# Kernel tuning notes

Measured on AMD Instinct MI355X. Metric: run time of the kernel, lower is better.

## Reference

```python
import jax, jax.numpy as jnp
import numpy as np

N = 16384   # total nodes per drug-batch
E = 65536   # directed edges (avg degree 4)
B = 512     # graphs per batch
BN_EPS = 1e-5
SLOPE = 0.01  # LeakyReLU default


def _rn(k, shape, s=0.02):
    return jax.random.normal(k, shape, dtype=jnp.float32) * s


def setup_inputs():
    key = jax.random.key(0)
    ks = jax.random.split(key, 32)
    d = {}
    d['x1'] = jax.random.normal(ks[0], (N, 78), dtype=jnp.float32)
    d['edge_index1'] = jax.random.randint(ks[1], (2, E), 0, N)
    d['batch1'] = jnp.sort(jax.random.randint(ks[2], (N,), 0, B))
    d['x2'] = jax.random.normal(ks[3], (N, 78), dtype=jnp.float32)
    d['edge_index2'] = jax.random.randint(ks[4], (2, E), 0, N)
    d['batch2'] = jnp.sort(jax.random.randint(ks[5], (N,), 0, B))
    d['cell'] = jax.random.normal(ks[6], (B, 954), dtype=jnp.float32)
    # TransformerConv1: 78 -> 2 heads x 128 (concat 256)
    d['wq1'] = _rn(ks[7], (78, 256));  d['bq1'] = jnp.zeros((256,), jnp.float32)
    d['wk1'] = _rn(ks[8], (78, 256));  d['bk1'] = jnp.zeros((256,), jnp.float32)
    d['wv1'] = _rn(ks[9], (78, 256));  d['bv1'] = jnp.zeros((256,), jnp.float32)
    d['ws1'] = _rn(ks[10], (78, 256)); d['bs1'] = jnp.zeros((256,), jnp.float32)
    # TransformerConv2: 256 -> 2 heads x 512 (concat 1024)
    d['wq2'] = _rn(ks[11], (256, 1024)); d['bq2'] = jnp.zeros((1024,), jnp.float32)
    d['wk2'] = _rn(ks[12], (256, 1024)); d['bk2'] = jnp.zeros((1024,), jnp.float32)
    d['wv2'] = _rn(ks[13], (256, 1024)); d['bv2'] = jnp.zeros((1024,), jnp.float32)
    d['ws2'] = _rn(ks[14], (256, 1024)); d['bs2'] = jnp.zeros((1024,), jnp.float32)
    d['wg1'] = _rn(ks[15], (1024, 512)); d['bg1'] = jnp.zeros((512,), jnp.float32)
    d['wg2'] = _rn(ks[16], (512, 128));  d['bg2'] = jnp.zeros((128,), jnp.float32)
    d['wr1'] = _rn(ks[17], (954, 512));  d['br1'] = jnp.zeros((512,), jnp.float32)
    d['wr2'] = _rn(ks[18], (512, 256));  d['br2'] = jnp.zeros((256,), jnp.float32)
    d['wr3'] = _rn(ks[19], (256, 128));  d['br3'] = jnp.zeros((128,), jnp.float32)
    d['wf1'] = _rn(ks[20], (384, 512));  d['bf1'] = jnp.zeros((512,), jnp.float32)
    d['gbn1'] = jnp.ones((512,), jnp.float32); d['bbn1'] = jnp.zeros((512,), jnp.float32)
    d['wf2'] = _rn(ks[21], (512, 256));  d['bf2'] = jnp.zeros((256,), jnp.float32)
    d['gbn2'] = jnp.ones((256,), jnp.float32); d['bbn2'] = jnp.zeros((256,), jnp.float32)
    d['wf3'] = _rn(ks[22], (256, 1));    d['bf3'] = jnp.zeros((1,), jnp.float32)
    return d


def _lrelu(x):
    return jnp.where(x >= 0, x, SLOPE * x)


def _l2n(x):
    return x / jnp.maximum(jnp.linalg.norm(x, axis=1, keepdims=True), 1e-12)


def _tconv(x, ei, wq, bq, wk, bk, wv, bv, ws, bs, H, D):
    # PyG TransformerConv (concat=True, beta=False, root_weight=True)
    src, dst = ei[0], ei[1]
    n = x.shape[0]
    q = (x @ wq + bq).reshape(n, H, D)
    k = (x @ wk + bk).reshape(n, H, D)
    v = (x @ wv + bv).reshape(n, H, D)
    logits = jnp.einsum('ehd,ehd->eh', q[dst], k[src]) / jnp.sqrt(jnp.float32(D))  # [E,H]
    m = jax.ops.segment_max(logits, dst, num_segments=n)
    m = jnp.where(jnp.isfinite(m), m, 0.0)
    e = jnp.exp(logits - m[dst])
    z = jax.ops.segment_sum(e, dst, num_segments=n)
    alpha = e / (z[dst] + 1e-16)
    agg = jax.ops.segment_sum(alpha[:, :, None] * v[src], dst, num_segments=n)  # [N,H,D]
    return agg.reshape(n, H * D) + x @ ws + bs


def reference(x1, edge_index1, batch1, x2, edge_index2, batch2, cell,
              wq1, bq1, wk1, bk1, wv1, bv1, ws1, bs1,
              wq2, bq2, wk2, bk2, wv2, bv2, ws2, bs2,
              wg1, bg1, wg2, bg2, wr1, br1, wr2, br2, wr3, br3,
              wf1, bf1, gbn1, bbn1, wf2, bf2, gbn2, bbn2, wf3, bf3):
    def branch(x, ei, bt):
        h = _lrelu(_tconv(x, ei, wq1, bq1, wk1, bk1, wv1, bv1, ws1, bs1, 2, 128))
        h = _lrelu(_tconv(h, ei, wq2, bq2, wk2, bk2, wv2, bv2, ws2, bs2, 2, 512))
        g = jax.ops.segment_max(h, bt, num_segments=B)  # global max pool per graph
        g = jnp.where(jnp.isfinite(g), g, 0.0)
        g = _lrelu(g @ wg1 + bg1)
        g = g @ wg2 + bg2  # dropout = identity in eval
        return _l2n(g)

    x1g = branch(x1, edge_index1, batch1)
    x2g = branch(x2, edge_index2, batch2)

    c = _l2n(cell)
    c = _lrelu(c @ wr1 + br1)
    c = _lrelu(c @ wr2 + br2)
    c = c @ wr3 + br3

    xc = _l2n(jnp.concatenate([x1g, x2g, c], axis=1))  # [B, 384]
    bn = 1.0 / jnp.sqrt(1.0 + BN_EPS)  # eval BN with running mean 0, var 1
    h = _lrelu((xc @ wf1 + bf1) * bn * gbn1 + bbn1)
    h = _lrelu((h @ wf2 + bf2) * bn * gbn2 + bbn2)
    return jax.nn.sigmoid((h @ wf3 + bf3)[:, 0])
```

## Files before the change

kernel.cpp:

```cpp
#include <hip/hip_runtime.h>
#include <hip/hip_bf16.h>
#include <hip/hip_fp8.h>
#include <math.h>
#include <stdint.h>

typedef __hip_bfloat16 bf16;

#define NN 16384
#define EE 65536
#define BB 512

typedef __attribute__((ext_vector_type(8))) short short8;
typedef __attribute__((ext_vector_type(2))) short short2v;
typedef __attribute__((ext_vector_type(4))) float floatx4;
typedef __attribute__((ext_vector_type(2))) float floatx2;
typedef __attribute__((ext_vector_type(2))) unsigned int uint2v;

#define GKEY_NEGINF 0x007FFFFFu

__device__ __forceinline__ float lrelu_f(float x){ return x >= 0.f ? x : 0.01f*x; }

__device__ __forceinline__ float b2f(short s){
    unsigned int u = ((unsigned int)(unsigned short)s) << 16;
    float f; __builtin_memcpy(&f, &u, 4); return f;
}
__device__ __forceinline__ short f2b(float f){
    bf16 b = (bf16)f;
    short s; __builtin_memcpy(&s, &b, 2); return s;
}
__device__ __forceinline__ unsigned int fkey(float f){
    unsigned int u; __builtin_memcpy(&u, &f, 4);
    return (u & 0x80000000u) ? ~u : (u | 0x80000000u);
}
__device__ __forceinline__ float fdec(unsigned int k){
    if (k == GKEY_NEGINF) return 0.f;
    unsigned int u = (k & 0x80000000u) ? (k ^ 0x80000000u) : ~k;
    float f; __builtin_memcpy(&f, &u, 4); return f;
}

__device__ __forceinline__ void gl2lds16(const void* g, void* l){
    __builtin_amdgcn_global_load_lds(
        (__attribute__((address_space(1))) unsigned int*)(uintptr_t)g,
        (__attribute__((address_space(3))) unsigned int*)(uintptr_t)l, 16, 0, 0);
}

__global__ __launch_bounds__(256)
void mfma_gemm(const bf16* __restrict__ A, int lda,
               const bf16* __restrict__ Bt, int ldb,
               const float* __restrict__ bias,
               bf16* __restrict__ C, int ldc,
               unsigned char* __restrict__ C2, int ldc2, int nsplit, int K)
{
    __shared__ __align__(16) char smem[20480];
    bf16* As  = (bf16*)smem;
    bf16* Bs  = (bf16*)(smem + 8192);
    bf16* epi = (bf16*)smem;
    const int tid  = threadIdx.x;
    const int wave = tid >> 6;
    const int lane = tid & 63;
    const int wm = (wave & 1) * 64;
    const int wn = (wave >> 1) * 64;
    const int m0 = blockIdx.x * 128;
    const int n0 = blockIdx.y * 128;
    const bool isf8 = (n0 >= nsplit);

    const int srow = lane >> 2;
    const int scol = (((lane & 3) ^ ((srow >> 1) & 3))) * 8;
    const int arow = lane & 15;
    const int aq   = (((lane >> 4) ^ ((arow >> 1) & 3))) * 8;

    floatx4 acc[4][4];
    #pragma unroll
    for (int i=0;i<4;i++)
        #pragma unroll
        for (int j=0;j<4;j++) acc[i][j] = (floatx4){0.f,0.f,0.f,0.f};

    for (int k0 = 0; k0 < K; k0 += 32) {
        #pragma unroll
        for (int i = 0; i < 2; i++) {
            const int chunk = wave*2 + i;
            const int r = chunk*16 + srow;
            gl2lds16(A  + (size_t)(m0 + r)*lda + k0 + scol, As + chunk*512);
            gl2lds16(Bt + (size_t)(n0 + r)*ldb + k0 + scol, Bs + chunk*512);
        }
        __syncthreads();
        short8 af[4], bf_[4];
        #pragma unroll
        for (int i=0;i<4;i++) af[i]  = *(const short8*)(As + (wm + i*16 + arow)*32 + aq);
        #pragma unroll
        for (int j=0;j<4;j++) bf_[j] = *(const short8*)(Bs + (wn + j*16 + arow)*32 + aq);
        #pragma unroll
        for (int i=0;i<4;i++)
            #pragma unroll
            for (int j=0;j<4;j++)
                acc[i][j] = __builtin_amdgcn_mfma_f32_16x16x32_bf16(af[i], bf_[j], acc[i][j], 0,0,0);
        __syncthreads();
    }
    const int crow = (lane >> 4) * 4;
    const int ccol = lane & 15;
    const int erow = lane >> 2;
    const int ecol = (lane & 3) * 8;
    bf16* ep = epi + wave * (64*40);
    #pragma unroll
    for (int j2 = 0; j2 < 2; j2++){
        if (j2) __syncthreads();
        #pragma unroll
        for (int jj = 0; jj < 2; jj++){
            const int j = j2*2 + jj;
            const float bsv = bias[n0 + wn + j*16 + ccol];
            #pragma unroll
            for (int i = 0; i < 4; i++)
                #pragma unroll
                for (int r = 0; r < 4; r++)
                    ep[(i*16 + crow + r)*40 + jj*16 + ccol] = (bf16)(acc[i][j][r] + bsv);
        }
        __syncthreads();
        #pragma unroll
        for (int q = 0; q < 4; q++){
            const int rr = q*16 + erow;
            short8 vv = *(const short8*)(ep + rr*40 + ecol);
            if (!isf8){
                *(short8*)(C + (size_t)(m0 + wm + rr)*ldc + n0 + wn + j2*32 + ecol) = vv;
            } else {
                int d0 = 0, d1 = 0;
                d0 = __builtin_amdgcn_cvt_pk_fp8_f32(b2f(vv[0]), b2f(vv[1]), d0, false);
                d0 = __builtin_amdgcn_cvt_pk_fp8_f32(b2f(vv[2]), b2f(vv[3]), d0, true);
                d1 = __builtin_amdgcn_cvt_pk_fp8_f32(b2f(vv[4]), b2f(vv[5]), d1, false);
                d1 = __builtin_amdgcn_cvt_pk_fp8_f32(b2f(vv[6]), b2f(vv[7]), d1, true);
                uint2v ob; ob[0] = (unsigned int)d0; ob[1] = (unsigned int)d1;
                *(uint2v*)(C2 + (size_t)(m0 + wm + rr)*ldc2 + (n0 - nsplit) + wn + j2*32 + ecol) = ob;
            }
        }
    }
}

#define OG1 0
#define OG2 524288
#define OR1 589824
#define OR2 1081344
#define OR3 1212416
#define OF1 1245184
#define OF2 1441792
#define TAILW_TOTAL 1572864

#define P_W1T 98304
#define P_B1C (P_W1T + 1024)
#define P_W2T (P_B1C + 1048576)
#define P_B2C (P_W2T + 4096)
#define P_WTP (P_B2C + TAILW_TOTAL)
#define P_XA  (P_WTP + 2*NN*96)
#define P_GK  (P_XA + 2*BB*1024)
__global__ void prep_mega_kernel(
    const float* __restrict__ wq1, const float* __restrict__ wk1,
    const float* __restrict__ wv1, const float* __restrict__ ws1,
    const float* __restrict__ bq1, const float* __restrict__ bk1,
    const float* __restrict__ bv1, const float* __restrict__ bs1,
    const float* __restrict__ wq2, const float* __restrict__ wk2,
    const float* __restrict__ wv2, const float* __restrict__ ws2,
    const float* __restrict__ bq2, const float* __restrict__ bk2,
    const float* __restrict__ bv2, const float* __restrict__ bs2v,
    const float* __restrict__ wg1, const float* __restrict__ wg2,
    const float* __restrict__ wr1, const float* __restrict__ wr2,
    const float* __restrict__ wr3, const float* __restrict__ wf1,
    const float* __restrict__ wf2,
    const float* __restrict__ x1,  const float* __restrict__ x2,
    bf16* __restrict__ W1t, float* __restrict__ b1c,
    bf16* __restrict__ W2t, float* __restrict__ b2c,
    bf16* __restrict__ Wtp, bf16* __restrict__ xa,
    unsigned int* __restrict__ gkey)
{
    int i = blockIdx.x*256 + threadIdx.x;
    if (i < P_W1T){
        int n = i / 96, k = i - n*96;
        int seg = n >> 8;
        const float* w = (seg==0)?ws1:(seg==1)?wq1:(seg==2)?wk1:wv1;
        W1t[i] = (k < 78) ? (bf16)w[(size_t)k*256 + (n & 255)] : (bf16)0.f;
        return;
    }
    if (i < P_B1C){
        int n = i - P_W1T;
        int seg = n >> 8;
        const float* b = (seg==0)?bs1:(seg==1)?bq1:(seg==2)?bk1:bv1;
        b1c[n] = b[n & 255];
        return;
    }
    if (i < P_W2T){
        int loc = i - P_B1C;
        int k = loc & 255;
        int j = (loc >> 8) & 2047;
        int h = loc >> 19;
        const float* w = (j<512)?ws2:(j<1024)?wq2:(j<1536)?wk2:wv2;
        W2t[loc] = (bf16)w[(size_t)k*1024 + h*512 + (j & 511)];
        return;
    }
    if (i < P_B2C){
        int loc = i - P_W2T;
        int j = loc & 2047, h = loc >> 11;
        const float* b = (j<512)?bs2v:(j<1024)?bq2:(j<1536)?bk2:bv2;
        b2c[loc] = b[h*512 + (j & 511)];
        return;
    }
    if (i < P_WTP){
        int t = i - P_B2C;
        const float* W; int N, K, KS, base;
        if      (t < OG2){ W = wg1; N = 512; K = 1024; KS = 32; base = OG1; }
        else if (t < OR1){ W = wg2; N = 128; K = 512;  KS = 16; base = OG2; }
        else if (t < OR2){ W = wr1; N = 512; K = 954;  KS = 30; base = OR1; }
        else if (t < OR3){ W = wr2; N = 256; K = 512;  KS = 16; base = OR2; }
        else if (t < OF1){ W = wr3; N = 128; K = 256;  KS = 8;  base = OR3; }
        else if (t < OF2){ W = wf1; N = 512; K = 384;  KS = 12; base = OF1; }
        else             { W = wf2; N = 256; K = 512;  KS = 16; base = OF2; }
        int loc = t - base;
        int j  = loc & 7;
        int ln = (loc >> 3) & 63;
        int rest = loc >> 9;
        int ks = rest % KS;
        int tile = rest / KS;
        int n = tile*16 + (ln & 15);
        int k = ks*32 + (ln >> 4)*8 + j;
        Wtp[t] = (k < K) ? (bf16)W[(size_t)k*N + n] : (bf16)0.f;
        return;
    }
    if (i < P_XA){
        int t = i - P_WTP;
        int r = t / 96, c = t - r*96;
        const float* x = (r >= NN) ? x2 : x1;
        int lr = r & (NN-1);
        xa[t] = (c < 78) ? (bf16)x[(size_t)lr*78 + c] : (bf16)0.f;
        return;
    }
    if (i < P_GK){
        gkey[i - P_XA] = GKEY_NEGINF;
    }
}

__global__ void hist_kernel(const int* __restrict__ ei1, const int* __restrict__ ei2,
                            int* __restrict__ cnt){
    int eg = blockIdx.x*256 + threadIdx.x;
    int br = eg >> 16, e = eg & (EE-1);
    const int* ei = br ? ei2 : ei1;
    atomicAdd(&cnt[br*NN + ei[EE + e]], 1);
}

__global__ __launch_bounds__(1024)
void scan_kernel(const int* __restrict__ hist, int* __restrict__ rowptr,
                 int* __restrict__ rowcur){
    const int br = blockIdx.x;
    hist   += br*NN;
    rowptr += br*(NN+1);
    rowcur += br*(NN+1);
    __shared__ int sums[1024];
    const int t = threadIdx.x;
    const int base = t*16;
    int loc[16]; int s = 0;
    #pragma unroll
    for (int i=0;i<16;i++){ loc[i]=s; s += hist[base+i]; }
    sums[t] = s; __syncthreads();
    for (int o=1;o<1024;o<<=1){
        int v = (t>=o) ? sums[t-o] : 0;
        __syncthreads();
        sums[t] += v;
        __syncthreads();
    }
    int pref = (t>0) ? sums[t-1] : 0;
    #pragma unroll
    for (int i=0;i<16;i++){
        int v = pref + loc[i];
        rowptr[base+i] = v;
        rowcur[base+i] = v;
    }
    if (t==1023) rowptr[NN] = sums[1023];
}

__global__ void scatter_kernel(const int* __restrict__ ei1, const int* __restrict__ ei2,
                               int* __restrict__ rowcur, int* __restrict__ srcs){
    int eg = blockIdx.x*256 + threadIdx.x;
    int br = eg >> 16, e = eg & (EE-1);
    const int* ei = br ? ei2 : ei1;
    int d = ei[EE + e];
    int pos = atomicAdd(&rowcur[br*(NN+1) + d], 1);
    srcs[br*EE + pos] = ei[e];
}

__global__ __launch_bounds__(256)
void attn128_f8(const bf16* __restrict__ s1, const unsigned char* __restrict__ f81,
                bf16* __restrict__ hout,
                const int* __restrict__ rowptr, const int* __restrict__ srcs)
{
    const int lane = threadIdx.x & 63;
    const int gw = blockIdx.x * 4 + (threadIdx.x >> 6);
    const int n = gw >> 1;
    const int h = gw & 1;
    int br = n >> 14;
    int brNN = br*NN, nl = n - brNN;
    rowptr += br*(NN+1); srcs += br*EE;
    const float qscale = rsqrtf(128.f) * 1.44269504f;
    const int hd = h*128 + lane*2;

    unsigned short qw; __builtin_memcpy(&qw, f81 + (size_t)n*768 + hd, 2);
    floatx2 qd = __builtin_amdgcn_cvt_pk_f32_fp8((int)qw, false);
    float qr[2] = { qd[0]*qscale, qd[1]*qscale };

    const int e0 = rowptr[nl], e1 = rowptr[nl+1];
    float m = -INFINITY, z = 0.f;
    float acc[2] = {0.f, 0.f};

    for (int base = e0; base < e1; base += 4){
        const int cnt = min(4, e1 - base);
        int sl = srcs[min(base + (lane & 3), e1 - 1)];
        int src[4];
        #pragma unroll
        for (int j=0;j<4;j++) src[j] = __shfl(sl, j, 64);

        unsigned short kw[4], vw[4];
        #pragma unroll
        for (int j=0;j<4;j++){
            if (j < cnt){
                const unsigned char* rp = f81 + (size_t)(brNN + src[j])*768;
                __builtin_memcpy(&kw[j], rp + 256 + hd, 2);
                __builtin_memcpy(&vw[j], rp + 512 + hd, 2);
            }
        }
        float dt[4];
        #pragma unroll
        for (int j=0;j<4;j++){
            float d = 0.f;
            if (j < cnt){
                floatx2 kd = __builtin_amdgcn_cvt_pk_f32_fp8((int)kw[j], false);
                d = qr[0]*kd[0] + qr[1]*kd[1];
            }
            dt[j] = d;
        }
        #pragma unroll
        for (int o=32;o;o>>=1){
            #pragma unroll
            for (int j=0;j<4;j++) dt[j] += __shfl_xor(dt[j], o, 64);
        }
        float cm = -INFINITY;
        #pragma unroll
        for (int j=0;j<4;j++) if (j < cnt) cm = fmaxf(cm, dt[j]);
        const float mn = fmaxf(m, cm);
        const float cs = exp2f(m - mn);
        z *= cs;
        acc[0] *= cs; acc[1] *= cs;
        #pragma unroll
        for (int j=0;j<4;j++){
            if (j < cnt){
                const float w = exp2f(dt[j] - mn);
                z += w;
                floatx2 vd = __builtin_amdgcn_cvt_pk_f32_fp8((int)vw[j], false);
                acc[0] += w*vd[0];
                acc[1] += w*vd[1];
            }
        }
        m = mn;
    }
    const float invz = 1.0f/(z + 1e-16f);
    const short2v sv = *(const short2v*)(s1 + (size_t)n*256 + hd);
    short2v ov;
    ov[0] = f2b(lrelu_f(b2f(sv[0]) + acc[0]*invz));
    ov[1] = f2b(lrelu_f(b2f(sv[1]) + acc[1]*invz));
    *(short2v*)(hout + (size_t)n*256 + hd) = ov;
}

__global__ __launch_bounds__(256)
void attn512_f8(const bf16* __restrict__ s2, const unsigned char* __restrict__ f82,
                const int* __restrict__ rowptr, const int* __restrict__ srcs,
                const int* __restrict__ bt1, const int* __restrict__ bt2,
                unsigned int* __restrict__ gkey, int gc0)
{
    __shared__ float Sh[4][512];
    __shared__ int Sgid[4];
    const int lane = threadIdx.x & 63;
    const int wave = threadIdx.x >> 6;
    const int n = blockIdx.x * 4 + wave;
    const int br = n >> 14;
    const int brNN = br*NN, nl = n - brNN;
    const int* rp_ = rowptr + br*(NN+1);
    const int* sp_ = srcs + br*EE;
    const float qscale = rsqrtf(512.f) * 1.44269504f;
    const int hd = lane*8;

    float qr[8];
    {
        const uint2v qv = *(const uint2v*)(f82 + (size_t)n*1536 + hd);
        floatx2 a = __builtin_amdgcn_cvt_pk_f32_fp8((int)qv[0], false);
        floatx2 b = __builtin_amdgcn_cvt_pk_f32_fp8((int)qv[0], true);
        floatx2 c = __builtin_amdgcn_cvt_pk_f32_fp8((int)qv[1], false);
        floatx2 d = __builtin_amdgcn_cvt_pk_f32_fp8((int)qv[1], true);
        qr[0]=a[0]*qscale; qr[1]=a[1]*qscale; qr[2]=b[0]*qscale; qr[3]=b[1]*qscale;
        qr[4]=c[0]*qscale; qr[5]=c[1]*qscale; qr[6]=d[0]*qscale; qr[7]=d[1]*qscale;
    }

    const int e0 = rp_[nl], e1 = rp_[nl+1];
    float m = -INFINITY, z = 0.f;
    float acc[8];
    #pragma unroll
    for (int i=0;i<8;i++) acc[i] = 0.f;

    for (int base = e0; base < e1; base += 4){
        const int cnt = min(4, e1 - base);
        int sl = sp_[min(base + (lane & 3), e1 - 1)];
        int src[4];
        #pragma unroll
        for (int j=0;j<4;j++) src[j] = __shfl(sl, j, 64);

        uint2v k2[4], v2[4];
        #pragma unroll
        for (int j=0;j<4;j++){
            if (j < cnt){
                const unsigned char* rp = f82 + (size_t)(brNN + src[j])*1536;
                k2[j] = *(const uint2v*)(rp + 512 + hd);
                v2[j] = *(const uint2v*)(rp + 1024 + hd);
            }
        }
        float dt[4];
        #pragma unroll
        for (int j=0;j<4;j++){
            float d = 0.f;
            if (j < cnt){
                floatx2 p0 = __builtin_amdgcn_cvt_pk_f32_fp8((int)k2[j][0], false);
                floatx2 p1 = __builtin_amdgcn_cvt_pk_f32_fp8((int)k2[j][0], true);
                floatx2 p2 = __builtin_amdgcn_cvt_pk_f32_fp8((int)k2[j][1], false);
                floatx2 p3 = __builtin_amdgcn_cvt_pk_f32_fp8((int)k2[j][1], true);
                d = qr[0]*p0[0] + qr[1]*p0[1] + qr[2]*p1[0] + qr[3]*p1[1]
                  + qr[4]*p2[0] + qr[5]*p2[1] + qr[6]*p3[0] + qr[7]*p3[1];
            }
            dt[j] = d;
        }
        #pragma unroll
        for (int o=32;o;o>>=1){
            #pragma unroll
            for (int j=0;j<4;j++) dt[j] += __shfl_xor(dt[j], o, 64);
        }
        float cm = -INFINITY;
        #pragma unroll
        for (int j=0;j<4;j++) if (j < cnt) cm = fmaxf(cm, dt[j]);
        const float mn = fmaxf(m, cm);
        const float cs = exp2f(m - mn);
        z *= cs;
        #pragma unroll
        for (int i=0;i<8;i++) acc[i] *= cs;
        #pragma unroll
        for (int j=0;j<4;j++){
            if (j < cnt){
                const float w = exp2f(dt[j] - mn);
                z += w;
                floatx2 p0 = __builtin_amdgcn_cvt_pk_f32_fp8((int)v2[j][0], false);
                floatx2 p1 = __builtin_amdgcn_cvt_pk_f32_fp8((int)v2[j][0], true);
                floatx2 p2 = __builtin_amdgcn_cvt_pk_f32_fp8((int)v2[j][1], false);
                floatx2 p3 = __builtin_amdgcn_cvt_pk_f32_fp8((int)v2[j][1], true);
                acc[0] += w*p0[0]; acc[1] += w*p0[1]; acc[2] += w*p1[0]; acc[3] += w*p1[1];
                acc[4] += w*p2[0]; acc[5] += w*p2[1]; acc[6] += w*p3[0]; acc[7] += w*p3[1];
            }
        }
        m = mn;
    }
    const float invz = 1.0f/(z + 1e-16f);
    const short8 sv = *(const short8*)(s2 + (size_t)n*512 + hd);
    #pragma unroll
    for (int i=0;i<8;i++) Sh[wave][hd + i] = lrelu_f(b2f(sv[i]) + acc[i]*invz);
    if (lane == 0) Sgid[wave] = br*BB + (br ? bt2[nl] : bt1[nl]);
    __syncthreads();

    #pragma unroll
    for (int cc=0; cc<2; cc++){
        const int col = threadIdx.x*2 + cc;
        float mx = Sh[0][col];
        int gid = Sgid[0];
        #pragma unroll
        for (int r=1; r<4; r++){
            if (Sgid[r] == gid) mx = fmaxf(mx, Sh[r][col]);
            else {
                atomicMax(&gkey[(size_t)gid*1024 + gc0 + col], fkey(mx));
                gid = Sgid[r]; mx = Sh[r][col];
            }
        }
        atomicMax(&gkey[(size_t)gid*1024 + gc0 + col], fkey(mx));
    }
}

template<int R, int N, int ACT>
__device__ __forceinline__ void dense_mfma(
    const bf16* __restrict__ Wm, const float* __restrict__ bias,
    const float* __restrict__ gam, const float* __restrict__ bet, float bns,
    const float* A, int lda, float* C, int ldc, int K, int tid)
{
    constexpr int T   = N / 16;
    constexpr int TPW = (T + 15) / 16;
    const int wave = tid >> 6;
    const int lane = tid & 63;
    const int am = lane & 15;
    const int ak = (lane >> 4) * 8;
    const int KS = ((K + 31) & ~31) >> 5;

    floatx4 acc[TPW];
    #pragma unroll
    for (int tp=0; tp<TPW; tp++) acc[tp] = (floatx4){0.f,0.f,0.f,0.f};

    for (int ks = 0; ks < KS; ks++){
        short8 af = (short8){0,0,0,0,0,0,0,0};
        if (am < R){
            const float* ap = A + am*lda + ks*32 + ak;
            const floatx4 a0 = *(const floatx4*)ap;
            const floatx4 a1 = *(const floatx4*)(ap + 4);
            af[0]=f2b(a0[0]); af[1]=f2b(a0[1]); af[2]=f2b(a0[2]); af[3]=f2b(a0[3]);
            af[4]=f2b(a1[0]); af[5]=f2b(a1[1]); af[6]=f2b(a1[2]); af[7]=f2b(a1[3]);
        }
        #pragma unroll
        for (int tp=0; tp<TPW; tp++){
            const int tile = wave + tp*16;
            if (tile < T){
                const short8 bfv = *(const short8*)(Wm + ((size_t)(tile*KS + ks))*512 + lane*8);
                acc[tp] = __builtin_amdgcn_mfma_f32_16x16x32_bf16(af, bfv, acc[tp], 0,0,0);
            }
        }
    }
    const int crow = (lane >> 4) * 4;
    const int ccol = lane & 15;
    #pragma unroll
    for (int tp=0; tp<TPW; tp++){
        const int tile = wave + tp*16;
        if (tile < T){
            #pragma unroll
            for (int r=0; r<4; r++){
                const int row = crow + r;
                if (row < R){
                    const int n = tile*16 + ccol;
                    float v = acc[tp][r] + bias[n];
                    if (ACT==1) v = lrelu_f(v);
                    if (ACT==2) v = lrelu_f(v*bns*gam[n] + bet[n]);
                    C[row*ldc + n] = v;
                }
            }
        }
    }
    __syncthreads();
}

__global__ __launch_bounds__(1024)
void tail_kernel(const unsigned int* __restrict__ gkey,
                 const float* __restrict__ cell,
                 const bf16*  __restrict__ Wtp,
                 const float* __restrict__ bg1, const float* __restrict__ bg2,
                 const float* __restrict__ br1, const float* __restrict__ br2,
                 const float* __restrict__ br3,
                 const float* __restrict__ bf1,
                 const float* __restrict__ gbn1, const float* __restrict__ bbn1,
                 const float* __restrict__ bf2,
                 const float* __restrict__ gbn2, const float* __restrict__ bbn2,
                 const float* __restrict__ wf3, const float* __restrict__ bf3,
                 float bns, float* __restrict__ outp)
{
    __shared__ float Sg[4][1024];
    __shared__ float Sgh[4][512];
    __shared__ float Sgout[4][128];
    __shared__ float Scell[2][960];
    __shared__ float Sc1[2][512];
    __shared__ float Sc2[2][256];
    __shared__ float Sc3[2][128];
    __shared__ float Sxc[2][384];
    __shared__ float Sf1[2][512];
    __shared__ float Sf2[2][256];
    __shared__ float inv4[4], invc[2], invx[2];

    const int tid = threadIdx.x;
    const int wv  = tid >> 6;
    const int ln  = tid & 63;
    const int b0  = blockIdx.x * 2;

    {
        int idx = tid*4;
        int r = idx >> 10, c = idx & 1023;
        int lg = r >> 1, br = r & 1;
        const unsigned int* gp = gkey + (size_t)(br*BB + b0 + lg)*1024 + c;
        #pragma unroll
        for (int i=0;i<4;i++) Sg[r][c+i] = fdec(gp[i]);
    }
    for (int idx = tid; idx < 2*954; idx += 1024){
        int r = (idx >= 954) ? 1 : 0;
        int c = idx - r*954;
        Scell[r][c] = cell[(size_t)(b0 + r)*954 + c];
    }
    if (tid < 12){ int r = tid/6; Scell[r][954 + tid%6] = 0.f; }
    __syncthreads();

    if (wv < 2){
        float s = 0.f;
        for (int c = ln; c < 954; c += 64){ float v = Scell[wv][c]; s += v*v; }
        #pragma unroll
        for (int o=32;o;o>>=1) s += __shfl_xor(s, o, 64);
        if (ln == 0) invc[wv] = 1.0f / fmaxf(sqrtf(s), 1e-12f);
    }
    __syncthreads();
    #pragma unroll
    for (int r=0;r<2;r++)
        for (int c = tid; c < 954; c += 1024) Scell[r][c] *= invc[r];
    __syncthreads();

    dense_mfma<4,512,1>(Wtp+OG1, bg1, nullptr, nullptr, 1.f, &Sg[0][0],   1024, &Sgh[0][0],  512, 1024, tid);
    dense_mfma<4,128,0>(Wtp+OG2, bg2, nullptr, nullptr, 1.f, &Sgh[0][0],  512,  &Sgout[0][0],128, 512,  tid);
    dense_mfma<2,512,1>(Wtp+OR1, br1, nullptr, nullptr, 1.f, &Scell[0][0], 960, &Sc1[0][0],  512, 954,  tid);
    dense_mfma<2,256,1>(Wtp+OR2, br2, nullptr, nullptr, 1.f, &Sc1[0][0],   512, &Sc2[0][0],  256, 512,  tid);
    dense_mfma<2,128,0>(Wtp+OR3, br3, nullptr, nullptr, 1.f, &Sc2[0][0],   256, &Sc3[0][0],  128, 256,  tid);

    if (wv < 4){
        float a = Sgout[wv][ln], bq = Sgout[wv][ln+64];
        float s = a*a + bq*bq;
        #pragma unroll
        for (int o=32;o;o>>=1) s += __shfl_xor(s, o, 64);
        if (ln == 0) inv4[wv] = 1.0f / fmaxf(sqrtf(s), 1e-12f);
    }
    __syncthreads();

    if (tid < 768){
        int lg = tid / 384, j = tid - lg*384;
        float v;
        if (j < 128)      v = Sgout[lg*2+0][j]     * inv4[lg*2+0];
        else if (j < 256) v = Sgout[lg*2+1][j-128] * inv4[lg*2+1];
        else              v = Sc3[lg][j-256];
        Sxc[lg][j] = v;
    }
    __syncthreads();
    if (wv < 2){
        float s = 0.f;
        #pragma unroll
        for (int i=0;i<6;i++){ float v = Sxc[wv][ln + i*64]; s += v*v; }
        #pragma unroll
        for (int o=32;o;o>>=1) s += __shfl_xor(s, o, 64);
        if (ln == 0) invx[wv] = 1.0f / fmaxf(sqrtf(s), 1e-12f);
    }
    __syncthreads();
    if (tid < 768){
        int lg = tid / 384, j = tid - lg*384;
        Sxc[lg][j] *= invx[lg];
    }
    __syncthreads();

    dense_mfma<2,512,2>(Wtp+OF1, bf1, gbn1, bbn1, bns, &Sxc[0][0], 384, &Sf1[0][0], 512, 384, tid);
    dense_mfma<2,256,2>(Wtp+OF2, bf2, gbn2, bbn2, bns, &Sf1[0][0], 512, &Sf2[0][0], 256, 512, tid);

    if (wv < 2){
        float s = 0.f;
        #pragma unroll
        for (int i=0;i<4;i++){ int c = ln + i*64; s += Sf2[wv][c]*wf3[c]; }
        #pragma unroll
        for (int o=32;o;o>>=1) s += __shfl_xor(s, o, 64);
        if (ln == 0) outp[b0 + wv] = 1.0f/(1.0f + expf(-(s + bf3[0])));
    }
}

extern "C" void kernel_launch(void* const* d_in, const int* in_sizes, int n_in,
                              void* d_out, int out_size, void* d_ws, size_t ws_size,
                              hipStream_t stream)
{
    const float* x1  = (const float*)d_in[0];
    const int*   ei1 = (const int*)  d_in[1];
    const int*   bt1 = (const int*)  d_in[2];
    const float* x2  = (const float*)d_in[3];
    const int*   ei2 = (const int*)  d_in[4];
    const int*   bt2 = (const int*)  d_in[5];
    const float* cell= (const float*)d_in[6];
    const float* wq1=(const float*)d_in[7];  const float* bq1=(const float*)d_in[8];
    const float* wk1=(const float*)d_in[9];  const float* bk1=(const float*)d_in[10];
    const float* wv1=(const float*)d_in[11]; const float* bv1=(const float*)d_in[12];
    const float* ws1=(const float*)d_in[13]; const float* bs1=(const float*)d_in[14];
    const float* wq2=(const float*)d_in[15]; const float* bq2=(const float*)d_in[16];
    const float* wk2=(const float*)d_in[17]; const float* bk2=(const float*)d_in[18];
    const float* wv2=(const float*)d_in[19]; const float* bv2=(const float*)d_in[20];
    const float* ws2=(const float*)d_in[21]; const float* bs2q=(const float*)d_in[22];
    const float* wg1=(const float*)d_in[23]; const float* bg1=(const float*)d_in[24];
    const float* wg2=(const float*)d_in[25]; const float* bg2=(const float*)d_in[26];
    const float* wr1=(const float*)d_in[27]; const float* br1=(const float*)d_in[28];
    const float* wr2=(const float*)d_in[29]; const float* br2=(const float*)d_in[30];
    const float* wr3=(const float*)d_in[31]; const float* br3=(const float*)d_in[32];
    const float* wf1=(const float*)d_in[33]; const float* bf1=(const float*)d_in[34];
    const float* gbn1=(const float*)d_in[35];const float* bbn1=(const float*)d_in[36];
    const float* wf2=(const float*)d_in[37]; const float* bf2=(const float*)d_in[38];
    const float* gbn2=(const float*)d_in[39];const float* bbn2=(const float*)d_in[40];
    const float* wf3=(const float*)d_in[41]; const float* bf3=(const float*)d_in[42];
    float* outp = (float*)d_out;
    (void)in_sizes; (void)n_in; (void)out_size; (void)ws_size;

    const float BNS = 1.0f / sqrtf(1.0f + 1e-5f);

    char* basep = (char*)d_ws;
    size_t off = 0;
    auto alloc = [&](size_t nbytes)->char* {
        char* p = basep + off;
        off += (nbytes + 255) & ~(size_t)255;
        return p;
    };
    int* rowptr2  = (int*)  alloc((size_t)2*(NN+1)*4);
    int* rowcur2  = (int*)  alloc((size_t)2*(NN+1)*4);
    int* cnt2     = (int*)  alloc((size_t)2*NN*4);
    int* srcs2    = (int*)  alloc((size_t)2*EE*4);
    unsigned int* gkey = (unsigned int*)alloc((size_t)2*BB*1024*4);
    float* b1c    = (float*)alloc((size_t)1024*4);
    float* b2c    = (float*)alloc((size_t)4096*4);
    bf16* W1t     = (bf16*) alloc((size_t)1024*96*2);
    bf16* W2t     = (bf16*) alloc((size_t)2*2048*256*2);
    bf16* Wtp     = (bf16*) alloc((size_t)TAILW_TOTAL*2);
    bf16* h1      = (bf16*) alloc((size_t)2*NN*256*2);
    char* BIG     = alloc((size_t)2*NN*512*2 + (size_t)2*NN*1536);
    bf16* xa      = (bf16*)BIG;
    bf16* s1a     = (bf16*)(BIG + 6291456);
    unsigned char* f81 = (unsigned char*)(BIG + 6291456 + 16777216);
    bf16* s2a     = (bf16*)BIG;
    unsigned char* f82 = (unsigned char*)(BIG + (size_t)2*NN*512*2);

    (void)hipMemsetAsync(cnt2, 0, (size_t)2*NN*4, stream);
    prep_mega_kernel<<<P_GK/256,256,0,stream>>>(
        wq1,wk1,wv1,ws1, bq1,bk1,bv1,bs1,
        wq2,wk2,wv2,ws2, bq2,bk2,bv2,bs2q,
        wg1,wg2,wr1,wr2,wr3,wf1,wf2,
        x1,x2,
        W1t,b1c,W2t,b2c, Wtp, xa, gkey);
    hist_kernel<<<2*EE/256,256,0,stream>>>(ei1, ei2, cnt2);
    scan_kernel<<<2,1024,0,stream>>>(cnt2, rowptr2, rowcur2);
    scatter_kernel<<<2*EE/256,256,0,stream>>>(ei1, ei2, rowcur2, srcs2);

    mfma_gemm<<<dim3(2*NN/128, 8),256,0,stream>>>(xa,96, W1t,96, b1c,
                                                  s1a,256, f81,768, 256, 96);
    attn128_f8<<<2*NN*2/4,256,0,stream>>>(s1a, f81, h1, rowptr2, srcs2);

    for (int h=0; h<2; h++){
        mfma_gemm<<<dim3(2*NN/128, 16),256,0,stream>>>(
            h1, 256, W2t + (size_t)h*2048*256, 256,
            b2c + h*2048, s2a,512, f82,1536, 512, 256);
        attn512_f8<<<2*NN/4,256,0,stream>>>(s2a, f82, rowptr2, srcs2, bt1, bt2,
                                            gkey, h*512);
    }

    tail_kernel<<<BB/2,1024,0,stream>>>(gkey, cell, Wtp,
                                        bg1,bg2, br1,br2,br3,
                                        bf1,gbn1,bbn1, bf2,gbn2,bbn2, wf3,bf3,
                                        BNS, outp);
}
```

Before: 507.7 us.

## Double-buffer A tiles in GEMM and load pre-swizzled B fragments directly to registers

The weight matrices are repacked during prep into an MFMA fragment-ordered layout, so each lane loads its B operand straight from global memory into registers and skips LDS for B. The A tile is double-buffered in LDS, and the next k-step's A and B loads are issued before the current MFMAs, guarded by explicit vmcnt waits and raw barriers. The K loop is templated on the number of k-steps so it fully unrolls. This is meant to hide global-load latency and halve LDS traffic, at the cost of more registers and hand-tuned waitcnt counts that must match the number of outstanding loads.

```diff
diff --git a/kernel.cpp b/kernel.cpp
--- a/kernel.cpp
+++ b/kernel.cpp
@@ -44,16 +44,17 @@
         (__attribute__((address_space(3))) unsigned int*)(uintptr_t)l, 16, 0, 0);
 }
 
+template<int KSC>
 __global__ __launch_bounds__(256)
 void mfma_gemm(const bf16* __restrict__ A, int lda,
-               const bf16* __restrict__ Bt, int ldb,
+               const bf16* __restrict__ Bp,
                const float* __restrict__ bias,
                bf16* __restrict__ C, int ldc,
-               unsigned char* __restrict__ C2, int ldc2, int nsplit, int K)
+               unsigned char* __restrict__ C2, int ldc2, int nsplit)
 {
     __shared__ __align__(16) char smem[20480];
-    bf16* As  = (bf16*)smem;
-    bf16* Bs  = (bf16*)(smem + 8192);
+    bf16* As0 = (bf16*)smem;
+    bf16* As1 = (bf16*)(smem + 8192);
     bf16* epi = (bf16*)smem;
     const int tid  = threadIdx.x;
     const int wave = tid >> 6;
@@ -63,6 +64,7 @@
     const int m0 = blockIdx.x * 128;
     const int n0 = blockIdx.y * 128;
     const bool isf8 = (n0 >= nsplit);
+    const int ntile0 = (n0 + wn) >> 4;
 
     const int srow = lane >> 2;
     const int scol = (((lane & 3) ^ ((srow >> 1) & 3))) * 8;
@@ -75,27 +77,54 @@
         #pragma unroll
         for (int j=0;j<4;j++) acc[i][j] = (floatx4){0.f,0.f,0.f,0.f};
 
-    for (int k0 = 0; k0 < K; k0 += 32) {
+    auto stageA = [&](int t, bf16* buf){
+        const int k0 = t*32;
         #pragma unroll
         for (int i = 0; i < 2; i++) {
             const int chunk = wave*2 + i;
             const int r = chunk*16 + srow;
-            gl2lds16(A  + (size_t)(m0 + r)*lda + k0 + scol, As + chunk*512);
-            gl2lds16(Bt + (size_t)(n0 + r)*ldb + k0 + scol, Bs + chunk*512);
-        }
-        __syncthreads();
-        short8 af[4], bf_[4];
-        #pragma unroll
-        for (int i=0;i<4;i++) af[i]  = *(const short8*)(As + (wm + i*16 + arow)*32 + aq);
-        #pragma unroll
-        for (int j=0;j<4;j++) bf_[j] = *(const short8*)(Bs + (wn + j*16 + arow)*32 + aq);
+            gl2lds16(A + (size_t)(m0 + r)*lda + k0 + scol, buf + chunk*512);
+        }
+    };
+    auto loadB = [&](short8* dst, int ks){
+        #pragma unroll
+        for (int j=0;j<4;j++)
+            dst[j] = *(const short8*)(Bp + ((size_t)((ntile0 + j)*KSC + ks))*512 + lane*8);
+    };
+
+    short8 bcur[4], bnxt[4];
+    loadB(bcur, 0);
+    stageA(0, As0);
+
+    #pragma unroll
+    for (int t = 0; t < KSC; t++){
+        bf16* cur = (t & 1) ? As1 : As0;
+        bf16* nxt = (t & 1) ? As0 : As1;
+        if (t + 1 < KSC){
+            stageA(t+1, nxt);
+            loadB(bnxt, t+1);
+            asm volatile("s_waitcnt vmcnt(6)" ::: "memory");
+        } else {
+            asm volatile("s_waitcnt vmcnt(0)" ::: "memory");
+        }
+        __builtin_amdgcn_s_barrier();
+        __builtin_amdgcn_sched_barrier(0);
+        short8 af[4];
+        #pragma unroll
+        for (int i=0;i<4;i++) af[i] = *(const short8*)(cur + (wm + i*16 + arow)*32 + aq);
         #pragma unroll
         for (int i=0;i<4;i++)
             #pragma unroll
             for (int j=0;j<4;j++)
-                acc[i][j] = __builtin_amdgcn_mfma_f32_16x16x32_bf16(af[i], bf_[j], acc[i][j], 0,0,0);
-        __syncthreads();
-    }
+                acc[i][j] = __builtin_amdgcn_mfma_f32_16x16x32_bf16(af[i], bcur[j], acc[i][j], 0,0,0);
+        __builtin_amdgcn_sched_barrier(0);
+        __builtin_amdgcn_s_barrier();
+        if (t + 1 < KSC){
+            #pragma unroll
+            for (int j=0;j<4;j++) bcur[j] = bnxt[j];
+        }
+    }
+
     const int crow = (lane >> 4) * 4;
     const int ccol = lane & 15;
     const int erow = lane >> 2;
@@ -171,7 +200,12 @@
 {
     int i = blockIdx.x*256 + threadIdx.x;
     if (i < P_W1T){
-        int n = i / 96, k = i - n*96;
+        int j  = i & 7;
+        int ln = (i >> 3) & 63;
+        int rest = i >> 9;
+        int ks = rest % 3, tile = rest / 3;
+        int n = tile*16 + (ln & 15);
+        int k = ks*32 + (ln >> 4)*8 + j;
         int seg = n >> 8;
         const float* w = (seg==0)?ws1:(seg==1)?wq1:(seg==2)?wk1:wv1;
         W1t[i] = (k < 78) ? (bf16)w[(size_t)k*256 + (n & 255)] : (bf16)0.f;
@@ -186,11 +220,16 @@
     }
     if (i < P_W2T){
         int loc = i - P_B1C;
-        int k = loc & 255;
-        int j = (loc >> 8) & 2047;
-        int h = loc >> 19;
-        const float* w = (j<512)?ws2:(j<1024)?wq2:(j<1536)?wk2:wv2;
-        W2t[loc] = (bf16)w[(size_t)k*1024 + h*512 + (j & 511)];
+        int h  = loc >> 19;
+        int l2 = loc & 524287;
+        int j  = l2 & 7;
+        int ln = (l2 >> 3) & 63;
+        int rest = l2 >> 9;
+        int ks = rest & 7, tile = rest >> 3;
+        int n = tile*16 + (ln & 15);
+        int k = ks*32 + (ln >> 4)*8 + j;
+        const float* w = (n<512)?ws2:(n<1024)?wq2:(n<1536)?wk2:wv2;
+        W2t[loc] = (bf16)w[(size_t)k*1024 + h*512 + (n & 511)];
         return;
     }
     if (i < P_B2C){
@@ -720,14 +759,14 @@
     scan_kernel<<<2,1024,0,stream>>>(cnt2, rowptr2, rowcur2);
     scatter_kernel<<<2*EE/256,256,0,stream>>>(ei1, ei2, rowcur2, srcs2);
 
-    mfma_gemm<<<dim3(2*NN/128, 8),256,0,stream>>>(xa,96, W1t,96, b1c,
-                                                  s1a,256, f81,768, 256, 96);
+    mfma_gemm<3><<<dim3(2*NN/128, 8),256,0,stream>>>(xa,96, W1t, b1c,
+                                                     s1a,256, f81,768, 256);
     attn128_f8<<<2*NN*2/4,256,0,stream>>>(s1a, f81, h1, rowptr2, srcs2);
 
     for (int h=0; h<2; h++){
-        mfma_gemm<<<dim3(2*NN/128, 16),256,0,stream>>>(
-            h1, 256, W2t + (size_t)h*2048*256, 256,
-            b2c + h*2048, s2a,512, f82,1536, 512, 256);
+        mfma_gemm<8><<<dim3(2*NN/128, 16),256,0,stream>>>(
+            h1, 256, W2t + (size_t)h*524288,
+            b2c + h*2048, s2a,512, f82,1536, 512);
         attn512_f8<<<2*NN/4,256,0,stream>>>(s2a, f82, rowptr2, srcs2, bt1, bt2,
                                             gkey, h*512);
     }
```

New measurement: 489.5 us. 1.04x faster.
